# Kernel tuning notes

Measured on AMD Instinct MI355X. Metric: run time of the kernel, lower is better.

Reference implementation:

```python
import jax, jax.numpy as jnp
import numpy as np

N_FFT = 2048
STRIDE = 512
PAD = N_FFT // 2  # center padding removed at the end
B = 4
T = 512  # number of spectrogram frames


def _make_kernels():
    n = np.arange(N_FFT)
    # ang[out_sample, freq_bin] = 2*pi*n*k/N  (create_fourier_kernels, freq_scale='no', freq_bins=n_fft)
    ang = 2.0 * np.pi * np.outer(n, n) / N_FFT
    kernel_cos = np.cos(ang).astype(np.float32)
    kernel_sin = np.sin(ang).astype(np.float32)
    # scipy.signal.get_window('hann', N, fftbins=True) -> periodic hann
    window = (0.5 - 0.5 * np.cos(2.0 * np.pi * n / N_FFT)).astype(np.float32)
    return kernel_cos, kernel_sin, window


def setup_inputs() -> dict:
    key = jax.random.key(0)
    X = jax.random.normal(key, (B, N_FFT, T, 2), dtype=jnp.float32)
    kc, ks, w = _make_kernels()
    return {
        "X": X,
        "kernel_cos": jnp.asarray(kc),
        "kernel_sin": jnp.asarray(ks),
        "window": jnp.asarray(w),
    }


def reference(X, kernel_cos, kernel_sin, window):
    # X: (B, n_fft, T, 2) complex spectrogram (onesided=False)
    b, n_fft, t, _ = X.shape
    Xr = X[..., 0]
    Xi = X[..., 1]
    # inverse DFT via dense matmul against sinusoidal kernels (conv2d in torch):
    # frames[b, n, t] = sum_f Xr[b,f,t]*cos(2pi n f/N) - Xi[b,f,t]*sin(2pi n f/N)
    frames = (jnp.einsum('bft,nf->bnt', Xr, kernel_cos)
              - jnp.einsum('bft,nf->bnt', Xi, kernel_sin))
    frames = frames * window[None, :, None] / n_fft
    # overlap-add (torch fold): out[b, t*stride + n] += frames[b, n, t]
    out_len = n_fft + STRIDE * (t - 1)
    idx = (jnp.arange(n_fft)[:, None] + STRIDE * jnp.arange(t)[None, :]).reshape(-1)
    y = jnp.zeros((b, out_len), frames.dtype).at[:, idx].add(frames.reshape(b, -1))
    # window sum-square normalization (torch_window_sumsquare)
    w_sq = jnp.broadcast_to((window * window)[:, None], (n_fft, t)).reshape(-1)
    w_sum = jnp.zeros((out_len,), window.dtype).at[idx].add(w_sq)
    nonzero = w_sum > 1e-10
    denom = jnp.where(nonzero, w_sum, jnp.ones_like(w_sum))
    y = jnp.where(nonzero[None, :], y / denom[None, :], y)
    # center=True, length=None -> trim pad_amount from both ends
    return y[:, PAD:-PAD]
```

## Files before the change

### kernel.cpp

```cpp
#include <hip/hip_runtime.h>

#define NFFT 2048
#define TT   512
#define BB   4
#define OUTL 261632
#define OUTTOT (BB*OUTL)

__device__ __forceinline__ int sigA(int c) { return c ^ ((c >> 4) & 7); }
__device__ __forceinline__ int sig2(int c) { return c ^ (((c >> 6) & 1) << 3); }

__device__ __forceinline__ float2 cmul(float2 a, float2 w) {
    return make_float2(a.x * w.x - a.y * w.y, a.x * w.y + a.y * w.x);
}

__device__ __forceinline__ void dft8(const float2 a[8], float2 o[8]) {
    float e0r = a[0].x + a[4].x, e0i = a[0].y + a[4].y;
    float e1r = a[0].x - a[4].x, e1i = a[0].y - a[4].y;
    float e2r = a[2].x + a[6].x, e2i = a[2].y + a[6].y;
    float e3r = a[6].y - a[2].y, e3i = a[2].x - a[6].x;
    float E0r = e0r + e2r, E0i = e0i + e2i;
    float E1r = e1r + e3r, E1i = e1i + e3i;
    float E2r = e0r - e2r, E2i = e0i - e2i;
    float E3r = e1r - e3r, E3i = e1i - e3i;
    float f0r = a[1].x + a[5].x, f0i = a[1].y + a[5].y;
    float f1r = a[1].x - a[5].x, f1i = a[1].y - a[5].y;
    float f2r = a[3].x + a[7].x, f2i = a[3].y + a[7].y;
    float f3r = a[7].y - a[3].y, f3i = a[3].x - a[7].x;
    float O0r = f0r + f2r, O0i = f0i + f2i;
    float O1r = f1r + f3r, O1i = f1i + f3i;
    float O2r = f0r - f2r, O2i = f0i - f2i;
    float O3r = f1r - f3r, O3i = f1i - f3i;
    const float h = 0.70710678118654752f;
    float W1r = h * (O1r - O1i), W1i = h * (O1r + O1i);
    float W2r = -O2i,            W2i = O2r;
    float W3r = -h * (O3r + O3i), W3i = h * (O3r - O3i);
    o[0] = make_float2(E0r + O0r, E0i + O0i);
    o[1] = make_float2(E1r + W1r, E1i + W1i);
    o[2] = make_float2(E2r + W2r, E2i + W2i);
    o[3] = make_float2(E3r + W3r, E3i + W3i);
    o[4] = make_float2(E0r - O0r, E0i - O0i);
    o[5] = make_float2(E1r - W1r, E1i - W1i);
    o[6] = make_float2(E2r - W2r, E2i - W2i);
    o[7] = make_float2(E3r - W3r, E3i - W3i);
}

__device__ __forceinline__ void twpow8(float2 o[8], float2 w1) {
    float2 w2 = cmul(w1, w1);
    float2 w3 = cmul(w2, w1);
    float2 w4 = cmul(w2, w2);
    o[1] = cmul(o[1], w1);
    o[2] = cmul(o[2], w2);
    o[3] = cmul(o[3], w3);
    o[4] = cmul(o[4], w4);
    o[5] = cmul(o[5], cmul(w4, w1));
    o[6] = cmul(o[6], cmul(w4, w2));
    o[7] = cmul(o[7], cmul(w4, w3));
}

__global__ __launch_bounds__(256) void fft_k(const float* __restrict__ X,
                                             const float* __restrict__ kc,
                                             const float* __restrict__ ks,
                                             float* __restrict__ Ft) {
    __shared__ float2 buf[2048];
    __shared__ float2 twL[32];
    const int S = blockIdx.x;
    const int c = ((S & 7) << 8) + (((S >> 6) & 31) << 3) + ((S >> 3) & 7);
    const int b = c >> 9;
    const int t = c & 511;
    const int u = threadIdx.x;
    const float* tw_c = kc + 2048;
    const float* tw_s = ks + 2048;

    if (u < 32) twL[u] = make_float2(tw_c[u << 3], tw_s[u << 3]);

    const float* Xb = X + ((size_t)b * 2048 * 512 + t) * 2;
    float2 a[8], o[8];
    #pragma unroll
    for (int l = 0; l < 8; l++)
        a[l] = *reinterpret_cast<const float2*>(Xb + (size_t)(u + 256 * l) * 1024);
    dft8(a, o);
    twpow8(o, make_float2(tw_c[u], tw_s[u]));
    #pragma unroll
    for (int k = 0; k < 8; k++) buf[sigA(8 * u + k)] = o[k];
    __syncthreads();

    #pragma unroll
    for (int l = 0; l < 8; l++) a[l] = buf[sigA(u + 256 * l)];
    __syncthreads();
    dft8(a, o);
    twpow8(o, twL[u >> 3]);
    {
        int base = 64 * (u >> 3) + (u & 7);
        #pragma unroll
        for (int k = 0; k < 8; k++) buf[sig2(base + 8 * k)] = o[k];
    }
    __syncthreads();

    #pragma unroll
    for (int l = 0; l < 8; l++) a[l] = buf[sig2(u + 256 * l)];
    __syncthreads();
    dft8(a, o);
    twpow8(o, twL[(u >> 6) << 3]);
    {
        int base = 512 * (u >> 6) + (u & 63);
        #pragma unroll
        for (int k = 0; k < 8; k++) buf[base + 64 * k] = o[k];
    }
    __syncthreads();

    float* outp = Ft + (size_t)c * 2048;
    #pragma unroll
    for (int half = 0; half < 2; half++) {
        int uu = u + 256 * half;
        float2 d0 = buf[uu], d1 = buf[uu + 512], d2 = buf[uu + 1024], d3 = buf[uu + 1536];
        float t0 = d0.x + d2.x;
        float t1 = d0.x - d2.x;
        float t2 = d1.x + d3.x;
        float t3 = d3.y - d1.y;
        outp[uu]        = t0 + t2;
        outp[uu + 512]  = t1 + t3;
        outp[uu + 1024] = t0 - t2;
        outp[uu + 1536] = t1 - t3;
    }
}

__global__ __launch_bounds__(256) void ola_k(const float* __restrict__ Ft,
                                             const float* __restrict__ win,
                                             float* __restrict__ out) {
    int j1 = blockIdx.x * 256 + threadIdx.x;
    if (j1 >= OUTTOT) return;
    int b  = j1 / OUTL;
    int jp = j1 - b * OUTL;
    int j  = jp + 1024;
    int tbase = j >> 9;
    int r = j & 511;
    float acc = 0.f, ws = 0.f;
    #pragma unroll
    for (int k = 0; k < 4; k++) {
        int t = tbase - k;
        if (t >= 0 && t < TT) {
            int n = r + (k << 9);
            float w = win[n];
            acc += Ft[(size_t)(b * TT + t) * NFFT + n] * w;
            ws  += w * w;
        }
    }
    float y = acc * (1.0f / (float)NFFT);
    if (ws > 1e-10f) y /= ws;
    out[j1] = y;
}

extern "C" void kernel_launch(void* const* d_in, const int* in_sizes, int n_in,
                              void* d_out, int out_size, void* d_ws, size_t ws_size,
                              hipStream_t stream) {
    const float* X  = (const float*)d_in[0];
    const float* kc = (const float*)d_in[1];
    const float* ks = (const float*)d_in[2];
    const float* w  = (const float*)d_in[3];
    float* out = (float*)d_out;

    float* Ft = (float*)d_ws;

    fft_k<<<dim3(BB * TT), dim3(256), 0, stream>>>(X, kc, ks, Ft);
    ola_k<<<dim3((OUTTOT + 255) / 256), dim3(256), 0, stream>>>(Ft, w, out);
}
```

Measured before the change: 34.49 us.

## Batch eight frames per FFT block with coalesced float4 loads into shared tile

Each block now handles eight consecutive frames with 1024 threads. The input is loaded as float4 (two adjacent time frames per load) into a 128 KB shared tile with a rotating swizzle, replacing the strided 8-byte gathers. Four frames are transformed at a time by four 256-thread groups, looping twice, and twiddles come from a shared 256-entry table. This is meant to cut wasted global-memory bandwidth on the strided input reads. In exchange, the large shared allocation allows only one block per CU, there are fewer blocks overall (256), and the butterfly stages are serialized by extra barriers.

New measurement: 31.63 us. -8.3%, faster.

```diff
diff --git a/kernel.cpp b/kernel.cpp
--- a/kernel.cpp
+++ b/kernel.cpp
@@ -6,8 +6,9 @@
 #define OUTL 261632
 #define OUTTOT (BB*OUTL)
 
-__device__ __forceinline__ int sigA(int c) { return c ^ ((c >> 4) & 7); }
-__device__ __forceinline__ int sig2(int c) { return c ^ (((c >> 6) & 1) << 3); }
+__device__ __forceinline__ int TIDX(int i, int c) {
+    return i * 8 + ((c + i + (i >> 3)) & 7);
+}
 
 __device__ __forceinline__ float2 cmul(float2 a, float2 w) {
     return make_float2(a.x * w.x - a.y * w.y, a.x * w.y + a.y * w.x);
@@ -57,70 +58,86 @@
     o[7] = cmul(o[7], cmul(w4, w3));
 }
 
-__global__ __launch_bounds__(256) void fft_k(const float* __restrict__ X,
-                                             const float* __restrict__ kc,
-                                             const float* __restrict__ ks,
-                                             float* __restrict__ Ft) {
-    __shared__ float2 buf[2048];
-    __shared__ float2 twL[32];
-    const int S = blockIdx.x;
-    const int c = ((S & 7) << 8) + (((S >> 6) & 31) << 3) + ((S >> 3) & 7);
-    const int b = c >> 9;
-    const int t = c & 511;
-    const int u = threadIdx.x;
-    const float* tw_c = kc + 2048;
-    const float* tw_s = ks + 2048;
+__global__ __launch_bounds__(1024) void fft_k(const float* __restrict__ X,
+                                              const float* __restrict__ kc,
+                                              const float* __restrict__ ks,
+                                              float* __restrict__ Ft) {
+    __shared__ float2 tile[2048 * 8];
+    __shared__ float2 tw256[256];
 
-    if (u < 32) twL[u] = make_float2(tw_c[u << 3], tw_s[u << 3]);
+    const int S  = blockIdx.x;
+    const int c0 = S * 8;
+    const int b  = c0 >> 9;
+    const int t0 = c0 & 511;
+    const int tid = threadIdx.x;
 
-    const float* Xb = X + ((size_t)b * 2048 * 512 + t) * 2;
-    float2 a[8], o[8];
+    if (tid < 256)
+        tw256[tid] = make_float2(kc[2048 + tid], ks[2048 + tid]);
+
+    const float* Xb = X + ((size_t)b * 2048 * 512 + t0) * 2;
     #pragma unroll
-    for (int l = 0; l < 8; l++)
-        a[l] = *reinterpret_cast<const float2*>(Xb + (size_t)(u + 256 * l) * 1024);
-    dft8(a, o);
-    twpow8(o, make_float2(tw_c[u], tw_s[u]));
-    #pragma unroll
-    for (int k = 0; k < 8; k++) buf[sigA(8 * u + k)] = o[k];
-    __syncthreads();
-
-    #pragma unroll
-    for (int l = 0; l < 8; l++) a[l] = buf[sigA(u + 256 * l)];
-    __syncthreads();
-    dft8(a, o);
-    twpow8(o, twL[u >> 3]);
-    {
-        int base = 64 * (u >> 3) + (u & 7);
-        #pragma unroll
-        for (int k = 0; k < 8; k++) buf[sig2(base + 8 * k)] = o[k];
+    for (int m = 0; m < 8; m++) {
+        int f = m * 256 + (tid >> 2);
+        int c = (tid & 3) * 2;
+        const float4 v = *reinterpret_cast<const float4*>(Xb + ((size_t)f * 512 + c) * 2);
+        tile[TIDX(f, c)]     = make_float2(v.x, v.y);
+        tile[TIDX(f, c + 1)] = make_float2(v.z, v.w);
     }
     __syncthreads();
 
-    #pragma unroll
-    for (int l = 0; l < 8; l++) a[l] = buf[sig2(u + 256 * l)];
-    __syncthreads();
-    dft8(a, o);
-    twpow8(o, twL[(u >> 6) << 3]);
-    {
-        int base = 512 * (u >> 6) + (u & 63);
+    const int g = tid >> 8;
+    const int u = tid & 255;
+    #pragma unroll 1
+    for (int r = 0; r < 2; r++) {
+        const int c = r * 4 + g;
+        float2 a[8], o[8];
         #pragma unroll
-        for (int k = 0; k < 8; k++) buf[base + 64 * k] = o[k];
-    }
-    __syncthreads();
-
-    float* outp = Ft + (size_t)c * 2048;
-    #pragma unroll
-    for (int half = 0; half < 2; half++) {
-        int uu = u + 256 * half;
-        float2 d0 = buf[uu], d1 = buf[uu + 512], d2 = buf[uu + 1024], d3 = buf[uu + 1536];
-        float t0 = d0.x + d2.x;
-        float t1 = d0.x - d2.x;
-        float t2 = d1.x + d3.x;
-        float t3 = d3.y - d1.y;
-        outp[uu]        = t0 + t2;
-        outp[uu + 512]  = t1 + t3;
-        outp[uu + 1024] = t0 - t2;
-        outp[uu + 1536] = t1 - t3;
+        for (int l = 0; l < 8; l++) a[l] = tile[TIDX(u + 256 * l, c)];
+        __syncthreads();
+        dft8(a, o);
+        twpow8(o, tw256[u]);
+        #pragma unroll
+        for (int k = 0; k < 8; k++) tile[TIDX(8 * u + k, c)] = o[k];
+        __syncthreads();
+        #pragma unroll
+        for (int l = 0; l < 8; l++) a[l] = tile[TIDX(u + 256 * l, c)];
+        __syncthreads();
+        dft8(a, o);
+        twpow8(o, tw256[u & ~7]);
+        {
+            int base = 64 * (u >> 3) + (u & 7);
+            #pragma unroll
+            for (int k = 0; k < 8; k++) tile[TIDX(base + 8 * k, c)] = o[k];
+        }
+        __syncthreads();
+        #pragma unroll
+        for (int l = 0; l < 8; l++) a[l] = tile[TIDX(u + 256 * l, c)];
+        __syncthreads();
+        dft8(a, o);
+        twpow8(o, tw256[u & ~63]);
+        {
+            int base = 512 * (u >> 6) + (u & 63);
+            #pragma unroll
+            for (int k = 0; k < 8; k++) tile[TIDX(base + 64 * k, c)] = o[k];
+        }
+        __syncthreads();
+        float* outp = Ft + (size_t)(c0 + c) * 2048;
+        #pragma unroll
+        for (int half = 0; half < 2; half++) {
+            int uu = u + 256 * half;
+            float2 d0 = tile[TIDX(uu, c)];
+            float2 d1 = tile[TIDX(uu + 512, c)];
+            float2 d2 = tile[TIDX(uu + 1024, c)];
+            float2 d3 = tile[TIDX(uu + 1536, c)];
+            float p0 = d0.x + d2.x;
+            float p1 = d0.x - d2.x;
+            float p2 = d1.x + d3.x;
+            float p3 = d3.y - d1.y;
+            outp[uu]        = p0 + p2;
+            outp[uu + 512]  = p1 + p3;
+            outp[uu + 1024] = p0 - p2;
+            outp[uu + 1536] = p1 - p3;
+        }
     }
 }
 
@@ -161,6 +178,6 @@
 
     float* Ft = (float*)d_ws;
 
-    fft_k<<<dim3(BB * TT), dim3(256), 0, stream>>>(X, kc, ks, Ft);
+    fft_k<<<dim3(BB * TT / 8), dim3(1024), 0, stream>>>(X, kc, ks, Ft);
     ola_k<<<dim3((OUTTOT + 255) / 256), dim3(256), 0, stream>>>(Ft, w, out);
 }
```
